# Optimization experiments

Hardware: AMD Instinct MI355X
Metric: run time of the kernel (lower is better)

The kernel has to match this reference:

```python
import jax, jax.numpy as jnp
import numpy as np

N, E = 50000, 800000
DIM, H, D = 256, 16, 8          # dim, num_heads, qk_dim
DH = D * H                      # 128
IN_RPE = 18
SCALE = D ** -0.5               # default qk_scale (None -> 1/sqrt(qk_dim))
EPS = 1e-16                     # torch_geometric softmax denominator eps


def setup_inputs() -> dict:
    key = jax.random.key(0)
    ks = jax.random.split(key, 10)
    x = jax.random.normal(ks[0], (N, DIM), dtype=jnp.float32)
    edge_index = jax.random.randint(ks[1], (2, E), 0, N, dtype=jnp.int64)
    edge_attr = jax.random.normal(ks[2], (E, IN_RPE), dtype=jnp.float32)
    # qkv Linear(dim -> 2*D*H + dim)
    Wqkv = jax.random.normal(ks[3], (DIM, 2 * DH + DIM), dtype=jnp.float32) * DIM ** -0.5
    bqkv = jnp.zeros((2 * DH + DIM,), dtype=jnp.float32)
    # k_rpe / q_rpe Linear(in_rpe_dim -> D*H) (heads_share_rpe=False)
    Wk_rpe = jax.random.normal(ks[4], (IN_RPE, DH), dtype=jnp.float32) * IN_RPE ** -0.5
    bk_rpe = jnp.zeros((DH,), dtype=jnp.float32)
    Wq_rpe = jax.random.normal(ks[5], (IN_RPE, DH), dtype=jnp.float32) * IN_RPE ** -0.5
    bq_rpe = jnp.zeros((DH,), dtype=jnp.float32)
    return {"x": x, "edge_index": edge_index, "edge_attr": edge_attr,
            "Wqkv": Wqkv, "bqkv": bqkv,
            "Wk_rpe": Wk_rpe, "bk_rpe": bk_rpe,
            "Wq_rpe": Wq_rpe, "bq_rpe": bq_rpe}


def _segment_softmax(compat, s, num_nodes):
    # numerically-stable softmax over edges grouped by source node s; compat: (E,H)
    m = jax.ops.segment_max(compat, s, num_segments=num_nodes)   # (N,H)
    ex = jnp.exp(compat - m[s])
    den = jax.ops.segment_sum(ex, s, num_segments=num_nodes)     # (N,H)
    return ex / (den[s] + EPS)


def reference(x, edge_index, edge_attr, Wqkv, bqkv, Wk_rpe, bk_rpe, Wq_rpe, bq_rpe):
    n = x.shape[0]
    e = edge_index.shape[1]
    qkv = x @ Wqkv + bqkv                      # (N, 2*DH + DIM)
    q = qkv[:, :DH].reshape(n, H, D)
    k = qkv[:, DH:2 * DH].reshape(n, H, D)
    v = qkv[:, 2 * DH:].reshape(n, H, DIM // H)
    s, t = edge_index[0], edge_index[1]
    qe = q[s] * SCALE                          # (E,H,D)
    ke = k[t]
    ke = ke + (edge_attr @ Wk_rpe + bk_rpe).reshape(e, H, D)
    qe = qe + (edge_attr @ Wq_rpe + bq_rpe).reshape(e, H, D)
    compat = jnp.einsum('ehd,ehd->eh', qe, ke)  # (E,H)
    attn = _segment_softmax(compat, s, n)       # (E,H)
    msg = (v[t] * attn[..., None]).reshape(e, DIM)  # (E,DIM)
    out = jax.ops.segment_sum(msg, s, num_segments=n)  # (N,DIM)
    return out
```

## Files before the change

### kernel.cpp

```cpp
#include <hip/hip_runtime.h>
#include <math.h>

#define DIMX   256
#define HEADS  16
#define QKD    8
#define DH     128
#define QKVW   512
#define INRPE  18
#define SCALE  0.35355339059327373f

__global__ __launch_bounds__(256) void qkv_gemm(
    const float* __restrict__ x, const float* __restrict__ W,
    const float* __restrict__ bias, float* __restrict__ qkv, int Nn)
{
    __shared__ float As[16][132];
    __shared__ float Bs[16][132];

    int tid  = threadIdx.x;
    int row0 = blockIdx.x * 128;
    int col0 = blockIdx.y * 128;
    int tx = tid & 15, ty = tid >> 4;

    float acc[8][8] = {};

    for (int k0 = 0; k0 < DIMX; k0 += 16) {
        #pragma unroll
        for (int r = 0; r < 2; r++) {
            int idx  = tid + r * 256;
            int arow = idx >> 2, acol = (idx & 3) * 4;
            float4 av = make_float4(0.f, 0.f, 0.f, 0.f);
            int grow = row0 + arow;
            if (grow < Nn) av = *(const float4*)&x[(size_t)grow * DIMX + k0 + acol];
            As[acol + 0][arow] = av.x;
            As[acol + 1][arow] = av.y;
            As[acol + 2][arow] = av.z;
            As[acol + 3][arow] = av.w;
        }
        #pragma unroll
        for (int r = 0; r < 2; r++) {
            int idx  = tid + r * 256;
            int brow = idx >> 5, bcol = (idx & 31) * 4;
            float4 bv = *(const float4*)&W[(size_t)(k0 + brow) * QKVW + col0 + bcol];
            *(float4*)&Bs[brow][bcol] = bv;
        }
        __syncthreads();
        #pragma unroll
        for (int kk = 0; kk < 16; kk++) {
            float a0[8], b0[8];
            *(float4*)&a0[0] = *(const float4*)&As[kk][ty * 8];
            *(float4*)&a0[4] = *(const float4*)&As[kk][ty * 8 + 4];
            *(float4*)&b0[0] = *(const float4*)&Bs[kk][tx * 4];
            *(float4*)&b0[4] = *(const float4*)&Bs[kk][64 + tx * 4];
            #pragma unroll
            for (int i = 0; i < 8; i++)
                #pragma unroll
                for (int j = 0; j < 8; j++)
                    acc[i][j] = fmaf(a0[i], b0[j], acc[i][j]);
        }
        __syncthreads();
    }

    float4 bv0 = *(const float4*)&bias[col0 + tx * 4];
    float4 bv1 = *(const float4*)&bias[col0 + 64 + tx * 4];
    float sc = (col0 == 0) ? SCALE : 1.0f;
    #pragma unroll
    for (int i = 0; i < 8; i++) {
        int grow = row0 + ty * 8 + i;
        if (grow < Nn) {
            float4 o0, o1;
            o0.x = (acc[i][0] + bv0.x) * sc;
            o0.y = (acc[i][1] + bv0.y) * sc;
            o0.z = (acc[i][2] + bv0.z) * sc;
            o0.w = (acc[i][3] + bv0.w) * sc;
            o1.x = (acc[i][4] + bv1.x) * sc;
            o1.y = (acc[i][5] + bv1.y) * sc;
            o1.z = (acc[i][6] + bv1.z) * sc;
            o1.w = (acc[i][7] + bv1.w) * sc;
            *(float4*)&qkv[(size_t)grow * QKVW + col0 + tx * 4] = o0;
            *(float4*)&qkv[(size_t)grow * QKVW + col0 + 64 + tx * 4] = o1;
        }
    }
}

__global__ void count_kernel(const int* __restrict__ ei, int* __restrict__ deg, int E)
{
    int e = blockIdx.x * blockDim.x + threadIdx.x;
    if (e < E) atomicAdd(&deg[ei[e]], 1);
}

__global__ __launch_bounds__(1024) void scan_kernel(
    const int* __restrict__ deg, int* __restrict__ off, int n)
{
    __shared__ int part[1024];
    int tid = threadIdx.x;
    int chunk = (n + 1023) / 1024;
    int s = tid * chunk;
    int epos = min(s + chunk, n);
    int sum = 0;
    for (int i = s; i < epos; i++) sum += deg[i];
    part[tid] = sum;
    __syncthreads();
    for (int d = 1; d < 1024; d <<= 1) {
        int v = (tid >= d) ? part[tid - d] : 0;
        __syncthreads();
        part[tid] += v;
        __syncthreads();
    }
    int run = part[tid] - sum;
    for (int i = s; i < epos; i++) { off[i] = run; run += deg[i]; }
    if (tid == 1023) off[n] = run;
}

__global__ void scatter_kernel(const int* __restrict__ ei,
                               const int* __restrict__ off, int* __restrict__ cur,
                               int2* __restrict__ elist, int E)
{
    int e = blockIdx.x * blockDim.x + threadIdx.x;
    if (e < E) {
        int s = ei[e];
        int t = ei[E + e];
        int pos = atomicAdd(&cur[s], 1);
        elist[off[s] + pos] = make_int2(e, t);
    }
}

__global__ __launch_bounds__(64, 3) void node_attn(
    const float* __restrict__ qkv, const int2* __restrict__ elist,
    const int* __restrict__ off, const float* __restrict__ edge_attr,
    const float* __restrict__ Wq_rpe, const float* __restrict__ bq_rpe,
    const float* __restrict__ Wk_rpe, const float* __restrict__ bk_rpe,
    float* __restrict__ out, int Nn)
{
    int lane = threadIdx.x;
    int n = blockIdx.x;
    if (n >= Nn) return;

    int c0 = lane * 2;

    float2 wq[INRPE], wk[INRPE];
    #pragma unroll
    for (int j = 0; j < INRPE; j++) {
        wq[j] = *(const float2*)&Wq_rpe[j * DH + c0];
        wk[j] = *(const float2*)&Wk_rpe[j * DH + c0];
    }
    float2 bq = *(const float2*)&bq_rpe[c0];
    float2 bk = *(const float2*)&bk_rpe[c0];

    float2 qs = *(const float2*)&qkv[(size_t)n * QKVW + c0];

    int beg = off[n], end = off[n + 1];

    float lsum = 0.0f;
    float4 o = make_float4(0.f, 0.f, 0.f, 0.f);

    #pragma unroll 2
    for (int i = beg; i < end; i++) {
        int2 et = elist[i];
        int e = et.x, t = et.y;

        float2 kt = *(const float2*)&qkv[(size_t)t * QKVW + DH + c0];
        float4 vt = *(const float4*)&qkv[(size_t)t * QKVW + 2 * DH + 4 * lane];

        const float2* ea2 = (const float2*)(edge_attr + (size_t)e * INRPE);
        float2 qr = bq, kr = bk;
        #pragma unroll
        for (int j = 0; j < 9; j++) {
            float2 av = ea2[j];
            qr.x = fmaf(av.x, wq[2 * j].x, qr.x);
            qr.y = fmaf(av.x, wq[2 * j].y, qr.y);
            kr.x = fmaf(av.x, wk[2 * j].x, kr.x);
            kr.y = fmaf(av.x, wk[2 * j].y, kr.y);
            qr.x = fmaf(av.y, wq[2 * j + 1].x, qr.x);
            qr.y = fmaf(av.y, wq[2 * j + 1].y, qr.y);
            kr.x = fmaf(av.y, wk[2 * j + 1].x, kr.x);
            kr.y = fmaf(av.y, wk[2 * j + 1].y, kr.y);
        }

        float c2 = (qs.x + qr.x) * (kt.x + kr.x) + (qs.y + qr.y) * (kt.y + kr.y);
        c2 += __shfl_xor(c2, 1, 64);
        c2 += __shfl_xor(c2, 2, 64);

        float ex = __expf(c2);
        lsum += ex;
        o.x = fmaf(ex, vt.x, o.x);
        o.y = fmaf(ex, vt.y, o.y);
        o.z = fmaf(ex, vt.z, o.z);
        o.w = fmaf(ex, vt.w, o.w);
    }

    float inv = 1.0f / (lsum + 1e-16f);
    float4 r = make_float4(o.x * inv, o.y * inv, o.z * inv, o.w * inv);
    *(float4*)&out[(size_t)n * DIMX + 4 * lane] = r;
}

extern "C" void kernel_launch(void* const* d_in, const int* in_sizes, int n_in,
                              void* d_out, int out_size, void* d_ws, size_t ws_size,
                              hipStream_t stream)
{
    const float* x    = (const float*)d_in[0];
    const int*   ei   = (const int*)d_in[1];
    const float* ea   = (const float*)d_in[2];
    const float* Wqkv = (const float*)d_in[3];
    const float* bqkv = (const float*)d_in[4];
    const float* Wk   = (const float*)d_in[5];
    const float* bk   = (const float*)d_in[6];
    const float* Wq   = (const float*)d_in[7];
    const float* bq   = (const float*)d_in[8];

    int Nn = in_sizes[0] / DIMX;
    int E  = in_sizes[1] / 2;
    float* out = (float*)d_out;

    float* qkv  = (float*)d_ws;
    int*   deg  = (int*)d_ws + (size_t)Nn * QKVW;
    int*   cur  = deg + Nn;
    int*   off  = cur + Nn;
    int2*  elist = (int2*)(off + ((Nn + 2) & ~1));

    hipMemsetAsync(deg, 0, sizeof(int) * 2 * (size_t)Nn, stream);

    qkv_gemm<<<dim3((Nn + 127) / 128, QKVW / 128), 256, 0, stream>>>(x, Wqkv, bqkv, qkv, Nn);
    count_kernel<<<(E + 255) / 256, 256, 0, stream>>>(ei, deg, E);
    scan_kernel<<<1, 1024, 0, stream>>>(deg, off, Nn);
    scatter_kernel<<<(E + 255) / 256, 256, 0, stream>>>(ei, off, cur, elist, E);
    node_attn<<<Nn, 64, 0, stream>>>(qkv, elist, off, ea, Wq, bq, Wk, bk, out, Nn);
}
```

Baseline: 689.5 us.

## Double-buffer QKV GEMM, warp-shuffle scan, widen node attention to 128 threads

The QKV GEMM now double-buffers its shared-memory tiles, prefetching the next k-slice into registers while the current one is computed. The offset scan is rebuilt as a chunked wave-shuffle scan with coalesced reads, replacing the per-thread serial chunks. Node attention moves to 128 threads per node, one q/k channel per thread, with an extra shuffle step so each 8-lane group reduces its own head. The wider block roughly halves per-thread work and register use in exchange for more threads, and a wavefront-uniform edge index is used to load edge attributes.

```diff
diff --git a/kernel.cpp b/kernel.cpp
--- a/kernel.cpp
+++ b/kernel.cpp
@@ -13,8 +13,8 @@
     const float* __restrict__ x, const float* __restrict__ W,
     const float* __restrict__ bias, float* __restrict__ qkv, int Nn)
 {
-    __shared__ float As[16][132];
-    __shared__ float Bs[16][132];
+    __shared__ float As[2][16][132];
+    __shared__ float Bs[2][16][132];
 
     int tid  = threadIdx.x;
     int row0 = blockIdx.x * 128;
@@ -22,41 +22,61 @@
     int tx = tid & 15, ty = tid >> 4;
 
     float acc[8][8] = {};
-
-    for (int k0 = 0; k0 < DIMX; k0 += 16) {
+    float4 a_reg[2], b_reg[2];
+
+    int a_row[2], a_col[2], b_row[2], b_col[2];
+    #pragma unroll
+    for (int r = 0; r < 2; r++) {
+        int idx = tid + r * 256;
+        a_row[r] = idx >> 2; a_col[r] = (idx & 3) * 4;
+        b_row[r] = idx >> 5; b_col[r] = (idx & 31) * 4;
+    }
+
+    auto load_tile = [&](int k0) {
         #pragma unroll
         for (int r = 0; r < 2; r++) {
-            int idx  = tid + r * 256;
-            int arow = idx >> 2, acol = (idx & 3) * 4;
-            float4 av = make_float4(0.f, 0.f, 0.f, 0.f);
-            int grow = row0 + arow;
-            if (grow < Nn) av = *(const float4*)&x[(size_t)grow * DIMX + k0 + acol];
-            As[acol + 0][arow] = av.x;
-            As[acol + 1][arow] = av.y;
-            As[acol + 2][arow] = av.z;
-            As[acol + 3][arow] = av.w;
-        }
+            int grow = row0 + a_row[r];
+            a_reg[r] = make_float4(0.f, 0.f, 0.f, 0.f);
+            if (grow < Nn) a_reg[r] = *(const float4*)&x[(size_t)grow * DIMX + k0 + a_col[r]];
+        }
+        #pragma unroll
+        for (int r = 0; r < 2; r++)
+            b_reg[r] = *(const float4*)&W[(size_t)(k0 + b_row[r]) * QKVW + col0 + b_col[r]];
+    };
+    auto store_tile = [&](int buf) {
         #pragma unroll
         for (int r = 0; r < 2; r++) {
-            int idx  = tid + r * 256;
-            int brow = idx >> 5, bcol = (idx & 31) * 4;
-            float4 bv = *(const float4*)&W[(size_t)(k0 + brow) * QKVW + col0 + bcol];
-            *(float4*)&Bs[brow][bcol] = bv;
-        }
-        __syncthreads();
+            As[buf][a_col[r] + 0][a_row[r]] = a_reg[r].x;
+            As[buf][a_col[r] + 1][a_row[r]] = a_reg[r].y;
+            As[buf][a_col[r] + 2][a_row[r]] = a_reg[r].z;
+            As[buf][a_col[r] + 3][a_row[r]] = a_reg[r].w;
+        }
+        #pragma unroll
+        for (int r = 0; r < 2; r++)
+            *(float4*)&Bs[buf][b_row[r]][b_col[r]] = b_reg[r];
+    };
+
+    load_tile(0);
+    store_tile(0);
+    __syncthreads();
+
+    for (int t = 0; t < DIMX / 16; t++) {
+        int cur = t & 1;
+        if (t < DIMX / 16 - 1) load_tile((t + 1) * 16);
         #pragma unroll
         for (int kk = 0; kk < 16; kk++) {
             float a0[8], b0[8];
-            *(float4*)&a0[0] = *(const float4*)&As[kk][ty * 8];
-            *(float4*)&a0[4] = *(const float4*)&As[kk][ty * 8 + 4];
-            *(float4*)&b0[0] = *(const float4*)&Bs[kk][tx * 4];
-            *(float4*)&b0[4] = *(const float4*)&Bs[kk][64 + tx * 4];
+            *(float4*)&a0[0] = *(const float4*)&As[cur][kk][ty * 8];
+            *(float4*)&a0[4] = *(const float4*)&As[cur][kk][ty * 8 + 4];
+            *(float4*)&b0[0] = *(const float4*)&Bs[cur][kk][tx * 4];
+            *(float4*)&b0[4] = *(const float4*)&Bs[cur][kk][64 + tx * 4];
             #pragma unroll
             for (int i = 0; i < 8; i++)
                 #pragma unroll
                 for (int j = 0; j < 8; j++)
                     acc[i][j] = fmaf(a0[i], b0[j], acc[i][j]);
         }
+        if (t < DIMX / 16 - 1) store_tile(cur ^ 1);
         __syncthreads();
     }
 
@@ -91,24 +111,40 @@
 __global__ __launch_bounds__(1024) void scan_kernel(
     const int* __restrict__ deg, int* __restrict__ off, int n)
 {
-    __shared__ int part[1024];
+    __shared__ int wsum[16];
+    __shared__ int wbase[16];
+    __shared__ int tot;
     int tid = threadIdx.x;
-    int chunk = (n + 1023) / 1024;
-    int s = tid * chunk;
-    int epos = min(s + chunk, n);
-    int sum = 0;
-    for (int i = s; i < epos; i++) sum += deg[i];
-    part[tid] = sum;
-    __syncthreads();
-    for (int d = 1; d < 1024; d <<= 1) {
-        int v = (tid >= d) ? part[tid - d] : 0;
-        __syncthreads();
-        part[tid] += v;
-        __syncthreads();
-    }
-    int run = part[tid] - sum;
-    for (int i = s; i < epos; i++) { off[i] = run; run += deg[i]; }
-    if (tid == 1023) off[n] = run;
+    int lane = tid & 63, w = tid >> 6;
+    int carry = 0;
+    for (int base = 0; base < n; base += 1024) {
+        int idx = base + tid;
+        int v = (idx < n) ? deg[idx] : 0;
+        int acc = v;
+        #pragma unroll
+        for (int d = 1; d < 64; d <<= 1) {
+            int u = __shfl_up(acc, d, 64);
+            if (lane >= d) acc += u;
+        }
+        if (lane == 63) wsum[w] = acc;
+        __syncthreads();
+        if (tid < 16) {
+            int s = wsum[tid];
+            int a = s;
+            #pragma unroll
+            for (int d = 1; d < 16; d <<= 1) {
+                int u = __shfl_up(a, d, 64);
+                if (tid >= d) a += u;
+            }
+            wbase[tid] = a - s;
+            if (tid == 15) tot = a;
+        }
+        __syncthreads();
+        if (idx < n) off[idx] = carry + wbase[w] + (acc - v);
+        carry += tot;
+        __syncthreads();
+    }
+    if (tid == 0) off[n] = carry;
 }
 
 __global__ void scatter_kernel(const int* __restrict__ ei,
@@ -124,73 +160,65 @@
     }
 }
 
-__global__ __launch_bounds__(64, 3) void node_attn(
+__global__ __launch_bounds__(128, 3) void node_attn(
     const float* __restrict__ qkv, const int2* __restrict__ elist,
     const int* __restrict__ off, const float* __restrict__ edge_attr,
     const float* __restrict__ Wq_rpe, const float* __restrict__ bq_rpe,
     const float* __restrict__ Wk_rpe, const float* __restrict__ bk_rpe,
     float* __restrict__ out, int Nn)
 {
-    int lane = threadIdx.x;
+    int tid = threadIdx.x;
     int n = blockIdx.x;
     if (n >= Nn) return;
-
-    int c0 = lane * 2;
-
-    float2 wq[INRPE], wk[INRPE];
+    int lane = tid & 63;
+
+    float wq[INRPE], wk[INRPE];
     #pragma unroll
     for (int j = 0; j < INRPE; j++) {
-        wq[j] = *(const float2*)&Wq_rpe[j * DH + c0];
-        wk[j] = *(const float2*)&Wk_rpe[j * DH + c0];
-    }
-    float2 bq = *(const float2*)&bq_rpe[c0];
-    float2 bk = *(const float2*)&bk_rpe[c0];
-
-    float2 qs = *(const float2*)&qkv[(size_t)n * QKVW + c0];
+        wq[j] = *(volatile const float*)&Wq_rpe[j * DH + tid];
+        wk[j] = *(volatile const float*)&Wk_rpe[j * DH + tid];
+    }
+    float qs = qkv[(size_t)n * QKVW + tid] + bq_rpe[tid];
+    float bk = bk_rpe[tid];
 
     int beg = off[n], end = off[n + 1];
 
     float lsum = 0.0f;
-    float4 o = make_float4(0.f, 0.f, 0.f, 0.f);
+    float2 o = make_float2(0.f, 0.f);
 
     #pragma unroll 2
     for (int i = beg; i < end; i++) {
         int2 et = elist[i];
-        int e = et.x, t = et.y;
-
-        float2 kt = *(const float2*)&qkv[(size_t)t * QKVW + DH + c0];
-        float4 vt = *(const float4*)&qkv[(size_t)t * QKVW + 2 * DH + 4 * lane];
+        int t = et.y;
+        int e = __builtin_amdgcn_readfirstlane(et.x);
+
+        float  kt = qkv[(size_t)t * QKVW + DH + tid];
+        float2 vt = *(const float2*)&qkv[(size_t)t * QKVW + 2 * DH + 2 * tid];
 
         const float2* ea2 = (const float2*)(edge_attr + (size_t)e * INRPE);
-        float2 qr = bq, kr = bk;
+        float qr = 0.f, kr = bk;
         #pragma unroll
         for (int j = 0; j < 9; j++) {
             float2 av = ea2[j];
-            qr.x = fmaf(av.x, wq[2 * j].x, qr.x);
-            qr.y = fmaf(av.x, wq[2 * j].y, qr.y);
-            kr.x = fmaf(av.x, wk[2 * j].x, kr.x);
-            kr.y = fmaf(av.x, wk[2 * j].y, kr.y);
-            qr.x = fmaf(av.y, wq[2 * j + 1].x, qr.x);
-            qr.y = fmaf(av.y, wq[2 * j + 1].y, qr.y);
-            kr.x = fmaf(av.y, wk[2 * j + 1].x, kr.x);
-            kr.y = fmaf(av.y, wk[2 * j + 1].y, kr.y);
-        }
-
-        float c2 = (qs.x + qr.x) * (kt.x + kr.x) + (qs.y + qr.y) * (kt.y + kr.y);
+            qr = fmaf(av.x, wq[2 * j], qr);
+            kr = fmaf(av.x, wk[2 * j], kr);
+            qr = fmaf(av.y, wq[2 * j + 1], qr);
+            kr = fmaf(av.y, wk[2 * j + 1], kr);
+        }
+
+        float c2 = (qs + qr) * (kt + kr);
         c2 += __shfl_xor(c2, 1, 64);
         c2 += __shfl_xor(c2, 2, 64);
+        c2 += __shfl_xor(c2, 4, 64);
 
         float ex = __expf(c2);
         lsum += ex;
         o.x = fmaf(ex, vt.x, o.x);
         o.y = fmaf(ex, vt.y, o.y);
-        o.z = fmaf(ex, vt.z, o.z);
-        o.w = fmaf(ex, vt.w, o.w);
     }
 
     float inv = 1.0f / (lsum + 1e-16f);
-    float4 r = make_float4(o.x * inv, o.y * inv, o.z * inv, o.w * inv);
-    *(float4*)&out[(size_t)n * DIMX + 4 * lane] = r;
+    *(float2*)&out[(size_t)n * DIMX + 2 * tid] = make_float2(o.x * inv, o.y * inv);
 }
 
 extern "C" void kernel_launch(void* const* d_in, const int* in_sizes, int n_in,
@@ -223,5 +251,5 @@
     count_kernel<<<(E + 255) / 256, 256, 0, stream>>>(ei, deg, E);
     scan_kernel<<<1, 1024, 0, stream>>>(deg, off, Nn);
     scatter_kernel<<<(E + 255) / 256, 256, 0, stream>>>(ei, off, cur, elist, E);
-    node_attn<<<Nn, 64, 0, stream>>>(qkv, elist, off, ea, Wq, bq, Wk, bk, out, Nn);
-}
+    node_attn<<<Nn, 128, 0, stream>>>(qkv, elist, off, ea, Wq, bq, Wk, bk, out, Nn);
+}
```

Measured after the change: 861.7 us. 25.0% more time.
